# Kernel optimization log

Hardware: AMD Instinct MI355X
Metric: run time of the kernel (lower is better)

## Reference

```python
import jax, jax.numpy as jnp
import numpy as np
from jax import lax

DIM = 384
NUM_HEADS = 8
KV_NUM_HEADS = 2
REP = NUM_HEADS // KV_NUM_HEADS  # 4
KV_DIM = DIM * 2 // REP          # 192
EPS_LN = 1e-5
EPS_NORM = 1e-12


def _layernorm_channel(x, w, b):
    # WithBias LayerNorm over channel dim of NCHW tensor (matches to_3d -> LN(c) -> to_4d)
    mu = jnp.mean(x, axis=1, keepdims=True)
    var = jnp.var(x, axis=1, keepdims=True)
    return (x - mu) / jnp.sqrt(var + EPS_LN) * w[None, :, None, None] + b[None, :, None, None]


def _conv1x1(x, w):
    # w: [out, in] ; x: [b, in, h, w]
    return jnp.einsum('oi,bihw->bohw', w, x)


def _dwconv3x3(x, w):
    # depthwise 3x3, padding=1; w: [C, 1, 3, 3]
    C = x.shape[1]
    return lax.conv_general_dilated(
        x, w, window_strides=(1, 1), padding=((1, 1), (1, 1)),
        feature_group_count=C,
        dimension_numbers=('NCHW', 'OIHW', 'NCHW'))


def _l2norm(x):
    n = jnp.linalg.norm(x, axis=-1, keepdims=True)
    return x / jnp.maximum(n, EPS_NORM)


def setup_inputs() -> dict:
    key = jax.random.key(0)
    ks = jax.random.split(key, 8)
    b, h, w = 8, 128, 128
    scale1 = 1.0 / np.sqrt(DIM)
    return {
        'q': jax.random.normal(ks[0], (b, DIM, h, w), dtype=jnp.float32),
        'k': jax.random.normal(ks[1], (b, DIM, h, w), dtype=jnp.float32),
        'w_q': jax.random.normal(ks[2], (DIM, DIM), dtype=jnp.float32) * scale1,
        'w_kv': jax.random.normal(ks[3], (KV_DIM, DIM), dtype=jnp.float32) * scale1,
        'w_q_dw': jax.random.normal(ks[4], (DIM, 1, 3, 3), dtype=jnp.float32) * (1.0 / 3.0),
        'w_kv_dw': jax.random.normal(ks[5], (KV_DIM, 1, 3, 3), dtype=jnp.float32) * (1.0 / 3.0),
        'w_out': jax.random.normal(ks[6], (DIM, DIM), dtype=jnp.float32) * scale1,
        'temperature': jnp.ones((NUM_HEADS, 1, 1), dtype=jnp.float32),
        'lnq_w': jnp.ones((DIM,), dtype=jnp.float32),
        'lnq_b': jnp.zeros((DIM,), dtype=jnp.float32),
        'lnk_w': jnp.ones((DIM,), dtype=jnp.float32),
        'lnk_b': jnp.zeros((DIM,), dtype=jnp.float32),
    }


def reference(q, k, w_q, w_kv, w_q_dw, w_kv_dw, w_out, temperature,
              lnq_w, lnq_b, lnk_w, lnk_b):
    b, c, h, w = q.shape
    hw = h * w
    qn = _layernorm_channel(q, lnq_w, lnq_b)
    kn = _layernorm_channel(k, lnk_w, lnk_b)
    qp = _dwconv3x3(_conv1x1(qn, w_q), w_q_dw)          # [b, dim, h, w]
    kv = _dwconv3x3(_conv1x1(kn, w_kv), w_kv_dw)        # [b, 2*dim/rep, h, w]
    kk, vv = jnp.split(kv, 2, axis=1)                   # each [b, dim/rep, h, w]
    # reshape to heads: channel-attention layout [b, head, c_head, hw]
    qh = qp.reshape(b, NUM_HEADS, DIM // NUM_HEADS, hw)
    kh = kk.reshape(b, KV_NUM_HEADS, DIM // NUM_HEADS, hw)
    vh = vv.reshape(b, KV_NUM_HEADS, DIM // NUM_HEADS, hw)
    # GQA repeat kv heads (repeat_interleave on head dim)
    kh = jnp.repeat(kh, REP, axis=1)
    vh = jnp.repeat(vh, REP, axis=1)
    qh = _l2norm(qh)
    kh = _l2norm(kh)
    attn = jnp.einsum('bhck,bhdk->bhcd', qh, kh) * temperature[None]
    attn = jax.nn.softmax(attn, axis=-1)
    out = jnp.einsum('bhcd,bhdk->bhck', attn, vh)       # [b, head, c_head, hw]
    out = out.reshape(b, DIM, h, w)
    return _conv1x1(out, w_out)
```

## Files before the change

kernel.cpp:

```cpp
#include <hip/hip_runtime.h>
#include <math.h>


typedef unsigned short u16;
typedef unsigned int u32;
typedef short s16x8 __attribute__((ext_vector_type(8)));
typedef float f32x4 __attribute__((ext_vector_type(4)));

#define HW 16384
#define NB 8
#define CDIM 384
#define KVC 192

__device__ __forceinline__ float b2f(u16 u) {
  return __uint_as_float(((u32)u) << 16);
}
__device__ __forceinline__ u16 f2b(float f) {
  u32 u = __float_as_uint(f);
  u += 0x7fffu + ((u >> 16) & 1u);
  return (u16)(u >> 16);
}
__device__ __forceinline__ u32 pack2(float a, float c) {
  return (u32)f2b(a) | ((u32)f2b(c) << 16);
}

__global__ void k0_prep(const float* __restrict__ wq, const float* __restrict__ wkv,
                        const float* __restrict__ wo,
                        const float* __restrict__ lnqw, const float* __restrict__ lnqb,
                        const float* __restrict__ lnkw, const float* __restrict__ lnkb,
                        u16* __restrict__ wqp, float* __restrict__ rwsQ, float* __restrict__ biasQ,
                        u16* __restrict__ wkvp, float* __restrict__ rwsKV, float* __restrict__ biasKV,
                        u16* __restrict__ wop) {
  int r = blockIdx.x * 256 + threadIdx.x;
  if (r < 384) {
    float rs = 0.f, bs = 0.f;
    for (int i = 0; i < 384; ++i) {
      float wp = wq[r * 384 + i] * lnqw[i];
      u16 h = f2b(wp);
      rs += b2f(h);
      bs += wq[r * 384 + i] * lnqb[i];
      wqp[r * 384 + i] = h;
    }
    rwsQ[r] = rs; biasQ[r] = bs;
  } else if (r < 640) {
    int o = r - 384;
    if (o < 192) {
      float rs = 0.f, bs = 0.f;
      for (int i = 0; i < 384; ++i) {
        float wp = wkv[o * 384 + i] * lnkw[i];
        u16 h = f2b(wp);
        rs += b2f(h);
        bs += wkv[o * 384 + i] * lnkb[i];
        wkvp[o * 384 + i] = h;
      }
      rwsKV[o] = rs; biasKV[o] = bs;
    } else {
      for (int i = 0; i < 384; ++i) wkvp[o * 384 + i] = 0;
      rwsKV[o] = 0.f; biasKV[o] = 0.f;
    }
  } else {
    int o = r - 640;
    for (int i = 0; i < 384; ++i) wop[o * 384 + i] = f2b(wo[o * 384 + i]);
  }
}

template <int MODE, int WM, int WN, int MF, int NF>
__global__ __launch_bounds__(512, 4) void gemm_fused(const u16* __restrict__ A,
                                                     const void* __restrict__ Bsrc,
                                                     const float* __restrict__ rowsum,
                                                     const float* __restrict__ bias,
                                                     void* __restrict__ outv, int M) {
  __shared__ __align__(16) char smem[57344];
  u16*   tB    = (u16*)smem;
  float* sredS = (float*)(smem + 49152);
  float* sredQ = (float*)(smem + 53248);
  u16*   chB16 = (u16*)smem;
  float* chB32 = (float*)smem;
  __shared__ float muL[64], sdL[64];

  constexpr int M_TILE = WM * MF * 16;

  const int b = blockIdx.z;
  const int pt = ((blockIdx.x & 7) << 5) | (blockIdx.x >> 3);
  const int tid = threadIdx.x;
  const int w = tid >> 6, l = tid & 63;
  const int wm = (WN == 1) ? w : (w >> 1);
  const int wn = (WN == 1) ? 0 : (w & 1);
  const int lr = l & 15, lg = l >> 4;

  f32x4 acc[MF][NF] = {};

  if (MODE == 0) {
    const float* Bf = (const float*)Bsrc;
    const size_t fbase = (size_t)b * CDIM * HW + (size_t)pt * 64 + l;
    float v[48];
#pragma unroll
    for (int it = 0; it < 12; ++it)
#pragma unroll
      for (int j = 0; j < 4; ++j)
        v[it * 4 + j] = Bf[fbase + (size_t)(it * 32 + w * 4 + j) * HW];

    float s_ = 0.f, q_ = 0.f;
#pragma unroll
    for (int it = 0; it < 12; ++it) {
      float v0 = v[it * 4], v1 = v[it * 4 + 1], v2 = v[it * 4 + 2], v3 = v[it * 4 + 3];
      s_ += (v0 + v1) + (v2 + v3);
      q_ += (v0 * v0 + v1 * v1) + (v2 * v2 + v3 * v3);
      u32 lo = pack2(v0, v1), hi = pack2(v2, v3);
      int cidx = it * 4 + (w >> 1);
      int off = l * 384 + ((cidx ^ (l & 7)) << 3) + (w & 1) * 4;
      *(uint2*)&tB[off] = make_uint2(lo, hi);
    }
    sredS[w * 64 + l] = s_;
    sredQ[w * 64 + l] = q_;
  } else {
    const u16* Bh = (const u16*)Bsrc;
    uint4 v[6];
#pragma unroll
    for (int i = 0; i < 6; ++i) {
      int chunk = tid + i * 512;
      int row = chunk / 48, c = chunk % 48;
      v[i] = *(const uint4*)(Bh + ((size_t)(b * HW + pt * 64 + row)) * 384 + c * 8);
    }
#pragma unroll
    for (int i = 0; i < 6; ++i) {
      int chunk = tid + i * 512;
      int row = chunk / 48, c = chunk % 48;
      *(uint4*)&tB[row * 384 + ((c ^ (row & 7)) << 3)] = v[i];
    }
  }
  __syncthreads();

  if (MODE == 0) {
    if (tid < 64) {
      float s = 0.f, q2 = 0.f;
#pragma unroll
      for (int g = 0; g < 8; ++g) { s += sredS[g * 64 + tid]; q2 += sredQ[g * 64 + tid]; }
      float mn = s * (1.f / 384.f);
      float var = q2 * (1.f / 384.f) - mn * mn;
      muL[tid] = mn;
      sdL[tid] = rsqrtf(var + 1e-5f);
    }
    __syncthreads();
  }

  s16x8 a[2][MF], bb[2][NF];
  {
#pragma unroll
    for (int mf = 0; mf < MF; ++mf)
      a[0][mf] = *(const s16x8*)(A + (size_t)(wm * (MF * 16) + mf * 16 + lr) * 384 + lg * 8);
#pragma unroll
    for (int nf = 0; nf < NF; ++nf) {
      int row = wn * (NF * 16) + nf * 16 + lr;
      bb[0][nf] = *(const s16x8*)&tB[row * 384 + ((lg ^ (row & 7)) << 3)];
    }
  }
#pragma unroll
  for (int ks = 0; ks < 12; ++ks) {
    const int cur = ks & 1, nxt = cur ^ 1;
    if (ks < 11) {
      const int ko = (ks + 1) * 32 + lg * 8;
      const int cidx = (ks + 1) * 4 + lg;
#pragma unroll
      for (int mf = 0; mf < MF; ++mf)
        a[nxt][mf] = *(const s16x8*)(A + (size_t)(wm * (MF * 16) + mf * 16 + lr) * 384 + ko);
#pragma unroll
      for (int nf = 0; nf < NF; ++nf) {
        int row = wn * (NF * 16) + nf * 16 + lr;
        bb[nxt][nf] = *(const s16x8*)&tB[row * 384 + ((cidx ^ (row & 7)) << 3)];
      }
    }
#pragma unroll
    for (int mf = 0; mf < MF; ++mf)
#pragma unroll
      for (int nf = 0; nf < NF; ++nf)
        acc[mf][nf] = __builtin_amdgcn_mfma_f32_16x16x32_bf16(a[cur][mf], bb[cur][nf], acc[mf][nf], 0, 0, 0);
  }

  if (MODE == 0) {
    __syncthreads();
#pragma unroll
    for (int nf = 0; nf < NF; ++nf) {
      int prow = wn * (NF * 16) + nf * 16 + lr;
      float m_ = muL[prow], s_ = sdL[prow];
#pragma unroll
      for (int mf = 0; mf < MF; ++mf)
#pragma unroll
        for (int r = 0; r < 4; ++r) {
          int orow = wm * (MF * 16) + mf * 16 + lg * 4 + r;
          float v = s_ * (acc[mf][nf][r] - m_ * rowsum[orow]) + bias[orow];
          chB16[orow * 72 + prow] = f2b(v);
        }
    }
    __syncthreads();
    const int total = M_TILE * 8;
    for (int i = tid; i < total; i += 512) {
      int row = i >> 3, c8 = i & 7;
      uint4 v = *(const uint4*)&chB16[row * 72 + c8 * 8];
      *(uint4*)((u16*)outv + ((size_t)(b * M + row)) * HW + pt * 64 + c8 * 8) = v;
    }
  } else {
#pragma unroll
    for (int cc = 0; cc < 2; ++cc) {
      __syncthreads();
      if ((wm >> 2) == cc) {
#pragma unroll
        for (int nf = 0; nf < NF; ++nf) {
          int prow = wn * (NF * 16) + nf * 16 + lr;
#pragma unroll
          for (int mf = 0; mf < MF; ++mf)
#pragma unroll
            for (int r = 0; r < 4; ++r) {
              int orow_l = (wm & 3) * (MF * 16) + mf * 16 + lg * 4 + r;
              chB32[orow_l * 72 + prow] = acc[mf][nf][r];
            }
        }
      }
      __syncthreads();
      for (int i = tid; i < 192 * 16; i += 512) {
        int row = i >> 4, c4 = i & 15;
        uint4 v = *(const uint4*)&chB32[row * 72 + c4 * 4];
        *(uint4*)((float*)outv + ((size_t)(b * CDIM + cc * 192 + row)) * HW + pt * 64 + c4 * 4) = v;
      }
    }
  }
}

__global__ __launch_bounds__(256) void k4_dw(const u16* __restrict__ qp, const u16* __restrict__ kvp,
                                             const float* __restrict__ wqdw, const float* __restrict__ wkvdw,
                                             u16* __restrict__ qd, u16* __restrict__ kvd,
                                             float* __restrict__ rnq, float* __restrict__ rnk) {
  __shared__ u16 plane[16384];
  __shared__ float red[256];

  int c = blockIdx.x, b = blockIdx.y;
  int tid = threadIdx.x;
  const u16* in; u16* outb; const float* wp; int C;
  int isQ = (c < 384), cc = isQ ? c : c - 384;
  if (isQ) { in = qp; outb = qd; wp = wqdw + cc * 9; C = CDIM; }
  else     { in = kvp; outb = kvd; wp = wkvdw + cc * 9; C = KVC; }
  size_t base = ((size_t)(b * C + cc)) * HW;

  float w[9];
#pragma unroll
  for (int j = 0; j < 9; ++j) w[j] = wp[j];

  const uint4* gsrc = (const uint4*)(in + base);
  uint4* lplane = (uint4*)plane;
#pragma unroll
  for (int i = 0; i < 8; ++i) lplane[tid + i * 256] = gsrc[tid + i * 256];
  __syncthreads();

  uint4* gdst = (uint4*)(outb + base);
  float ns = 0.f;
#pragma unroll
  for (int it = 0; it < 8; ++it) {
    int idx = tid + it * 256;
    int y = idx >> 4, ox = idx & 15;
    int x0 = ox * 8;

    float r[3][10];
#pragma unroll
    for (int rr = 0; rr < 3; ++rr) {
      int yy = y + rr - 1;
      if ((unsigned)yy < 128u) {
        int rbase = yy * 128 + x0;
        r[rr][0] = (x0 > 0) ? b2f(plane[rbase - 1]) : 0.f;
        uint4 v = *(const uint4*)&plane[rbase];
        u32 ws[4] = {v.x, v.y, v.z, v.w};
#pragma unroll
        for (int j = 0; j < 4; ++j) {
          r[rr][1 + 2 * j] = b2f((u16)(ws[j] & 0xffff));
          r[rr][2 + 2 * j] = b2f((u16)(ws[j] >> 16));
        }
        r[rr][9] = (x0 < 120) ? b2f(plane[rbase + 8]) : 0.f;
      } else {
#pragma unroll
        for (int j = 0; j < 10; ++j) r[rr][j] = 0.f;
      }
    }

    u32 packed[4];
#pragma unroll
    for (int j = 0; j < 8; ++j) {
      float a = 0.f;
#pragma unroll
      for (int rr = 0; rr < 3; ++rr)
#pragma unroll
        for (int dx = 0; dx < 3; ++dx)
          a += w[rr * 3 + dx] * r[rr][j + dx];
      u16 h = f2b(a);
      float hv = b2f(h);
      ns += hv * hv;
      if (j & 1) packed[j >> 1] |= ((u32)h) << 16; else packed[j >> 1] = (u32)h;
    }
    gdst[idx] = make_uint4(packed[0], packed[1], packed[2], packed[3]);
  }

  red[tid] = ns;
  __syncthreads();
  for (int st = 128; st > 0; st >>= 1) {
    if (tid < st) red[tid] += red[tid + st];
    __syncthreads();
  }
  if (tid == 0) {
    float n = sqrtf(red[0]);
    float inv = 1.f / fmaxf(n, 1e-12f);
    if (isQ) rnq[b * 384 + cc] = inv;
    else if (cc < 96) rnk[b * 96 + cc] = inv;
  }
}

__global__ void k5b_vt(const u16* __restrict__ kvd, u16* __restrict__ vt) {
  int p = blockIdx.x * 256 + threadIdx.x;
  int b = blockIdx.y;
  size_t sb = ((size_t)(b * KVC + 96)) * HW + p;
  uint4* dv = (uint4*)vt + ((size_t)(b * HW + p)) * 12;
  for (int j8 = 0; j8 < 12; ++j8) {
    u32 w[4];
#pragma unroll
    for (int j = 0; j < 8; ++j) {
      u16 h = kvd[sb + (size_t)(j8 * 8 + j) * HW];
      if (j & 1) w[j >> 1] |= ((u32)h) << 16; else w[j >> 1] = (u32)h;
    }
    dv[j8] = make_uint4(w[0], w[1], w[2], w[3]);
  }
}

__global__ __launch_bounds__(256) void k6_qk(const u16* __restrict__ qd,
                                             const u16* __restrict__ kvd,
                                             float* __restrict__ spart) {
  int kc = blockIdx.x, h = blockIdx.y, b = blockIdx.z;
  int tid = threadIdx.x;
  int w = tid >> 6, l = tid & 63, lr = l & 15, lg = l >> 4;
  int g = h >> 2;
  int p0 = kc * 1024 + w * 256;

  f32x4 acc[3][3] = {};
  size_t qbase = ((size_t)(b * CDIM + h * 48 + lr)) * HW;
  size_t kbase = ((size_t)(b * KVC + g * 48 + lr)) * HW;

  for (int ks = 0; ks < 8; ++ks) {
    int pp = p0 + ks * 32 + lg * 8;
    s16x8 a[3], bb[3];
#pragma unroll
    for (int mi = 0; mi < 3; ++mi) a[mi] = *(const s16x8*)(qd + qbase + (size_t)mi * 16 * HW + pp);
#pragma unroll
    for (int ni = 0; ni < 3; ++ni) bb[ni] = *(const s16x8*)(kvd + kbase + (size_t)ni * 16 * HW + pp);
#pragma unroll
    for (int mi = 0; mi < 3; ++mi)
#pragma unroll
      for (int ni = 0; ni < 3; ++ni)
        acc[mi][ni] = __builtin_amdgcn_mfma_f32_16x16x32_bf16(a[mi], bb[ni], acc[mi][ni], 0, 0, 0);
  }

  size_t sb = ((size_t)((((b * 8 + h) * 16) + kc) * 4 + w)) * 2304;
#pragma unroll
  for (int mi = 0; mi < 3; ++mi)
#pragma unroll
    for (int ni = 0; ni < 3; ++ni)
#pragma unroll
      for (int r = 0; r < 4; ++r) {
        int c = mi * 16 + lg * 4 + r, d = ni * 16 + lr;
        spart[sb + c * 48 + d] = acc[mi][ni][r];
      }
}

__global__ void k7_sm(const float* __restrict__ spart, const float* __restrict__ temp,
                      const float* __restrict__ rnq, const float* __restrict__ rnk,
                      u16* __restrict__ ptil) {
  int h = blockIdx.x, b = blockIdx.y, tid = threadIdx.x;
  int g = h >> 2;
  __shared__ float S[2304];
  size_t base = ((size_t)((b * 8 + h) * 64)) * 2304;
  for (int e = tid; e < 2304; e += 64) {
    float s = 0.f;
    for (int j = 0; j < 64; ++j) s += spart[base + (size_t)j * 2304 + e];
    S[e] = s;
  }
  __syncthreads();
  if (tid < 48) {
    int c = tid;
    float sq = temp[h] * rnq[b * 384 + h * 48 + c];
    float mx = -1e30f;
    for (int d = 0; d < 48; ++d) {
      float v = S[c * 48 + d] * sq * rnk[b * 96 + g * 48 + d];
      mx = fmaxf(mx, v);
    }
    float sum = 0.f;
    for (int d = 0; d < 48; ++d) {
      float v = S[c * 48 + d] * sq * rnk[b * 96 + g * 48 + d];
      sum += __expf(v - mx);
    }
    float inv = 1.f / sum;
    u16* row = ptil + ((size_t)(b * 384 + h * 48 + c)) * 96;
    for (int dk = 0; dk < 96; ++dk) {
      int d = dk - g * 48;
      float pv = 0.f;
      if (d >= 0 && d < 48) {
        float v = S[c * 48 + d] * sq * rnk[b * 96 + g * 48 + d];
        pv = __expf(v - mx) * inv;
      }
      row[dk] = f2b(pv);
    }
  }
}

__global__ __launch_bounds__(512) void k8_pv(const u16* __restrict__ vt,
                                             const u16* __restrict__ ptil,
                                             u16* __restrict__ yt) {
  int ptb = blockIdx.x, b = blockIdx.y;
  int tid = threadIdx.x;
  int w = tid >> 6, l = tid & 63, lr = l & 15, lg = l >> 4;
  int wm = w >> 2, wn = w & 3;

  f32x4 acc[4][6] = {};
  size_t arow0 = ((size_t)(b * HW + ptb * 128 + wm * 64 + lr)) * 96;
  size_t brow0 = ((size_t)(b * CDIM + wn * 96 + lr)) * 96;

  for (int ks = 0; ks < 3; ++ks) {
    int ko = ks * 32 + lg * 8;
    s16x8 a[4], bb[6];
#pragma unroll
    for (int mf = 0; mf < 4; ++mf) a[mf] = *(const s16x8*)(vt + arow0 + (size_t)mf * 16 * 96 + ko);
#pragma unroll
    for (int nf = 0; nf < 6; ++nf) bb[nf] = *(const s16x8*)(ptil + brow0 + (size_t)nf * 16 * 96 + ko);
#pragma unroll
    for (int mf = 0; mf < 4; ++mf)
#pragma unroll
      for (int nf = 0; nf < 6; ++nf)
        acc[mf][nf] = __builtin_amdgcn_mfma_f32_16x16x32_bf16(a[mf], bb[nf], acc[mf][nf], 0, 0, 0);
  }

#pragma unroll
  for (int mf = 0; mf < 4; ++mf)
#pragma unroll
    for (int nf = 0; nf < 6; ++nf)
#pragma unroll
      for (int r = 0; r < 4; ++r) {
        int p = ptb * 128 + wm * 64 + mf * 16 + lg * 4 + r;
        int c = wn * 96 + nf * 16 + lr;
        yt[((size_t)(b * HW + p)) * 384 + c] = f2b(acc[mf][nf][r]);
      }
}

extern "C" void kernel_launch(void* const* d_in, const int* in_sizes, int n_in,
                              void* d_out, int out_size, void* d_ws, size_t ws_size,
                              hipStream_t stream) {
  const float* q    = (const float*)d_in[0];
  const float* k    = (const float*)d_in[1];
  const float* w_q  = (const float*)d_in[2];
  const float* w_kv = (const float*)d_in[3];
  const float* w_qd = (const float*)d_in[4];
  const float* w_kd = (const float*)d_in[5];
  const float* w_o  = (const float*)d_in[6];
  const float* temp = (const float*)d_in[7];
  const float* lnqw = (const float*)d_in[8];
  const float* lnqb = (const float*)d_in[9];
  const float* lnkw = (const float*)d_in[10];
  const float* lnkb = (const float*)d_in[11];
  float* out = (float*)d_out;

  char* ws = (char*)d_ws;
  size_t off = 0;
  auto alloc = [&](size_t bytes) -> void* {
    void* p = ws + off;
    off += (bytes + 255) & ~(size_t)255;
    return p;
  };

  u16*   wqp   = (u16*)alloc(384 * 384 * 2);
  float* rwsQ  = (float*)alloc(384 * 4);
  float* biasQ = (float*)alloc(384 * 4);
  u16*   wkvp  = (u16*)alloc(256 * 384 * 2);
  float* rwsKV = (float*)alloc(256 * 4);
  float* biasKV= (float*)alloc(256 * 4);
  u16*   wop   = (u16*)alloc(384 * 384 * 2);
  u16*   qp    = (u16*)alloc((size_t)NB * CDIM * HW * 2);
  u16*   kvp   = (u16*)alloc((size_t)NB * KVC * HW * 2);
  u16*   qd    = (u16*)alloc((size_t)NB * CDIM * HW * 2);
  u16*   kvd   = (u16*)alloc((size_t)NB * KVC * HW * 2);
  u16*   vt    = (u16*)alloc((size_t)NB * HW * 96 * 2);
  float* spart = (float*)alloc((size_t)4096 * 2304 * 4);
  u16*   ptil  = (u16*)alloc((size_t)NB * CDIM * 96 * 2);
  float* rnq   = (float*)alloc((size_t)NB * 384 * 4);
  float* rnk   = (float*)alloc((size_t)NB * 96 * 4);

  u16* yt = qp;

  k0_prep<<<4, 256, 0, stream>>>(w_q, w_kv, w_o, lnqw, lnqb, lnkw, lnkb,
                                 wqp, rwsQ, biasQ, wkvp, rwsKV, biasKV, wop);

  gemm_fused<0, 8, 1, 3, 4><<<dim3(256, 1, NB), 512, 0, stream>>>(wqp, q, rwsQ, biasQ, qp, 384);
  gemm_fused<0, 4, 2, 3, 2><<<dim3(256, 1, NB), 512, 0, stream>>>(wkvp, k, rwsKV, biasKV, kvp, 192);

  k4_dw<<<dim3(576, NB), 256, 0, stream>>>(qp, kvp, w_qd, w_kd, qd, kvd, rnq, rnk);

  k5b_vt<<<dim3(64, NB), 256, 0, stream>>>(kvd, vt);

  k6_qk<<<dim3(16, 8, NB), 256, 0, stream>>>(qd, kvd, spart);
  k7_sm<<<dim3(8, NB), 64, 0, stream>>>(spart, temp, rnq, rnk, ptil);

  k8_pv<<<dim3(128, NB), 512, 0, stream>>>(vt, ptil, yt);

  gemm_fused<1, 8, 1, 3, 4><<<dim3(256, 1, NB), 512, 0, stream>>>(wop, yt, nullptr, nullptr, out, 384);
}
```

Before: 620.3 us.

## Fuse PV product into output projection and merge Q/KV projection launches

The attention-times-V product is now computed per 64-pixel tile directly into shared memory and fed into the output 1x1 projection in the same kernel. This removes the bf16 round-trip of the intermediate yt tensor through global memory and one launch. The Q and KV projection GEMMs are merged into a single launch over 16 z-slices, with KV weights padded to 384 rows so both use the same tiling, which adds wasted MFMA work on zero rows for the KV half. The fused output kernel reloads the ptil rows from global per tile, and its larger shared-memory footprint may reduce occupancy.

Result: slower. 638.6 us (+3.0%).

```diff
diff --git a/kernel.cpp b/kernel.cpp
--- a/kernel.cpp
+++ b/kernel.cpp
@@ -42,7 +42,7 @@
       wqp[r * 384 + i] = h;
     }
     rwsQ[r] = rs; biasQ[r] = bs;
-  } else if (r < 640) {
+  } else if (r < 768) {
     int o = r - 384;
     if (o < 192) {
       float rs = 0.f, bs = 0.f;
@@ -58,40 +58,46 @@
       for (int i = 0; i < 384; ++i) wkvp[o * 384 + i] = 0;
       rwsKV[o] = 0.f; biasKV[o] = 0.f;
     }
-  } else {
-    int o = r - 640;
+  } else if (r < 1152) {
+    int o = r - 768;
     for (int i = 0; i < 384; ++i) wop[o * 384 + i] = f2b(wo[o * 384 + i]);
   }
 }
 
-template <int MODE, int WM, int WN, int MF, int NF>
-__global__ __launch_bounds__(512, 4) void gemm_fused(const u16* __restrict__ A,
-                                                     const void* __restrict__ Bsrc,
-                                                     const float* __restrict__ rowsum,
-                                                     const float* __restrict__ bias,
-                                                     void* __restrict__ outv, int M) {
-  __shared__ __align__(16) char smem[57344];
-  u16*   tB    = (u16*)smem;
-  float* sredS = (float*)(smem + 49152);
-  float* sredQ = (float*)(smem + 53248);
-  u16*   chB16 = (u16*)smem;
-  float* chB32 = (float*)smem;
-  __shared__ float muL[64], sdL[64];
-
-  constexpr int M_TILE = WM * MF * 16;
-
-  const int b = blockIdx.z;
+__global__ __launch_bounds__(512, 4) void gemm_qkv(const u16* __restrict__ Aq,
+                                                   const u16* __restrict__ Akv,
+                                                   const float* __restrict__ qsrc,
+                                                   const float* __restrict__ ksrc,
+                                                   const float* __restrict__ rwsQ,
+                                                   const float* __restrict__ biasQ,
+                                                   const float* __restrict__ rwsKV,
+                                                   const float* __restrict__ biasKV,
+                                                   u16* __restrict__ qp, u16* __restrict__ kvp) {
+  __shared__ __align__(16) char smem[53760];
+  u16*    tB   = (u16*)smem;
+  float2* sred = (float2*)(smem + 49152);
+  float*  muL  = (float*)(smem + 53248);
+  float*  sdL  = (float*)(smem + 53504);
+  u16*    chB16 = (u16*)smem;
+
+  const int zz = blockIdx.z;
+  const bool isQ = (zz < 8);
+  const int b = zz & 7;
+  const u16* A = isQ ? Aq : Akv;
+  const float* Bf = isQ ? qsrc : ksrc;
+  const float* rowsum = isQ ? rwsQ : rwsKV;
+  const float* bias = isQ ? biasQ : biasKV;
+  u16* outp = isQ ? qp : kvp;
+  const int M = isQ ? 384 : 192;
+
   const int pt = ((blockIdx.x & 7) << 5) | (blockIdx.x >> 3);
   const int tid = threadIdx.x;
   const int w = tid >> 6, l = tid & 63;
-  const int wm = (WN == 1) ? w : (w >> 1);
-  const int wn = (WN == 1) ? 0 : (w & 1);
   const int lr = l & 15, lg = l >> 4;
 
-  f32x4 acc[MF][NF] = {};
-
-  if (MODE == 0) {
-    const float* Bf = (const float*)Bsrc;
+  f32x4 acc[3][4] = {};
+
+  {
     const size_t fbase = (size_t)b * CDIM * HW + (size_t)pt * 64 + l;
     float v[48];
 #pragma unroll
@@ -111,49 +117,29 @@
       int off = l * 384 + ((cidx ^ (l & 7)) << 3) + (w & 1) * 4;
       *(uint2*)&tB[off] = make_uint2(lo, hi);
     }
-    sredS[w * 64 + l] = s_;
-    sredQ[w * 64 + l] = q_;
-  } else {
-    const u16* Bh = (const u16*)Bsrc;
-    uint4 v[6];
-#pragma unroll
-    for (int i = 0; i < 6; ++i) {
-      int chunk = tid + i * 512;
-      int row = chunk / 48, c = chunk % 48;
-      v[i] = *(const uint4*)(Bh + ((size_t)(b * HW + pt * 64 + row)) * 384 + c * 8);
-    }
-#pragma unroll
-    for (int i = 0; i < 6; ++i) {
-      int chunk = tid + i * 512;
-      int row = chunk / 48, c = chunk % 48;
-      *(uint4*)&tB[row * 384 + ((c ^ (row & 7)) << 3)] = v[i];
-    }
-  }
-  __syncthreads();
-
-  if (MODE == 0) {
-    if (tid < 64) {
-      float s = 0.f, q2 = 0.f;
-#pragma unroll
-      for (int g = 0; g < 8; ++g) { s += sredS[g * 64 + tid]; q2 += sredQ[g * 64 + tid]; }
-      float mn = s * (1.f / 384.f);
-      float var = q2 * (1.f / 384.f) - mn * mn;
-      muL[tid] = mn;
-      sdL[tid] = rsqrtf(var + 1e-5f);
-    }
-    __syncthreads();
-  }
-
-  s16x8 a[2][MF], bb[2][NF];
-  {
-#pragma unroll
-    for (int mf = 0; mf < MF; ++mf)
-      a[0][mf] = *(const s16x8*)(A + (size_t)(wm * (MF * 16) + mf * 16 + lr) * 384 + lg * 8);
-#pragma unroll
-    for (int nf = 0; nf < NF; ++nf) {
-      int row = wn * (NF * 16) + nf * 16 + lr;
-      bb[0][nf] = *(const s16x8*)&tB[row * 384 + ((lg ^ (row & 7)) << 3)];
-    }
+    sred[w * 64 + l] = make_float2(s_, q_);
+  }
+  __syncthreads();
+
+  if (tid < 64) {
+    float s = 0.f, q2 = 0.f;
+#pragma unroll
+    for (int g = 0; g < 8; ++g) { float2 t = sred[g * 64 + tid]; s += t.x; q2 += t.y; }
+    float mn = s * (1.f / 384.f);
+    float var = q2 * (1.f / 384.f) - mn * mn;
+    muL[tid] = mn;
+    sdL[tid] = rsqrtf(var + 1e-5f);
+  }
+  __syncthreads();
+
+  s16x8 a[2][3], bb[2][4];
+#pragma unroll
+  for (int mf = 0; mf < 3; ++mf)
+    a[0][mf] = *(const s16x8*)(A + (size_t)(w * 48 + mf * 16 + lr) * 384 + lg * 8);
+#pragma unroll
+  for (int nf = 0; nf < 4; ++nf) {
+    int row = nf * 16 + lr;
+    bb[0][nf] = *(const s16x8*)&tB[row * 384 + ((lg ^ (row & 7)) << 3)];
   }
 #pragma unroll
   for (int ks = 0; ks < 12; ++ks) {
@@ -162,65 +148,46 @@
       const int ko = (ks + 1) * 32 + lg * 8;
       const int cidx = (ks + 1) * 4 + lg;
 #pragma unroll
-      for (int mf = 0; mf < MF; ++mf)
-        a[nxt][mf] = *(const s16x8*)(A + (size_t)(wm * (MF * 16) + mf * 16 + lr) * 384 + ko);
-#pragma unroll
-      for (int nf = 0; nf < NF; ++nf) {
-        int row = wn * (NF * 16) + nf * 16 + lr;
+      for (int mf = 0; mf < 3; ++mf)
+        a[nxt][mf] = *(const s16x8*)(A + (size_t)(w * 48 + mf * 16 + lr) * 384 + ko);
+#pragma unroll
+      for (int nf = 0; nf < 4; ++nf) {
+        int row = nf * 16 + lr;
         bb[nxt][nf] = *(const s16x8*)&tB[row * 384 + ((cidx ^ (row & 7)) << 3)];
       }
     }
 #pragma unroll
-    for (int mf = 0; mf < MF; ++mf)
-#pragma unroll
-      for (int nf = 0; nf < NF; ++nf)
+    for (int mf = 0; mf < 3; ++mf)
+#pragma unroll
+      for (int nf = 0; nf < 4; ++nf)
         acc[mf][nf] = __builtin_amdgcn_mfma_f32_16x16x32_bf16(a[cur][mf], bb[cur][nf], acc[mf][nf], 0, 0, 0);
   }
 
-  if (MODE == 0) {
+#pragma unroll
+  for (int cc = 0; cc < 2; ++cc) {
     __syncthreads();
-#pragma unroll
-    for (int nf = 0; nf < NF; ++nf) {
-      int prow = wn * (NF * 16) + nf * 16 + lr;
-      float m_ = muL[prow], s_ = sdL[prow];
-#pragma unroll
-      for (int mf = 0; mf < MF; ++mf)
-#pragma unroll
-        for (int r = 0; r < 4; ++r) {
-          int orow = wm * (MF * 16) + mf * 16 + lg * 4 + r;
-          float v = s_ * (acc[mf][nf][r] - m_ * rowsum[orow]) + bias[orow];
-          chB16[orow * 72 + prow] = f2b(v);
-        }
+    if ((w >> 2) == cc) {
+#pragma unroll
+      for (int nf = 0; nf < 4; ++nf) {
+        int prow = nf * 16 + lr;
+        float m_ = muL[prow], s_ = sdL[prow];
+#pragma unroll
+        for (int mf = 0; mf < 3; ++mf)
+#pragma unroll
+          for (int r = 0; r < 4; ++r) {
+            int orow = w * 48 + mf * 16 + lg * 4 + r;
+            float v = s_ * (acc[mf][nf][r] - m_ * rowsum[orow]) + bias[orow];
+            chB16[((w & 3) * 48 + mf * 16 + lg * 4 + r) * 72 + prow] = f2b(v);
+          }
+      }
     }
     __syncthreads();
-    const int total = M_TILE * 8;
-    for (int i = tid; i < total; i += 512) {
+    for (int i = tid; i < 192 * 8; i += 512) {
       int row = i >> 3, c8 = i & 7;
-      uint4 v = *(const uint4*)&chB16[row * 72 + c8 * 8];
-      *(uint4*)((u16*)outv + ((size_t)(b * M + row)) * HW + pt * 64 + c8 * 8) = v;
-    }
-  } else {
-#pragma unroll
-    for (int cc = 0; cc < 2; ++cc) {
-      __syncthreads();
-      if ((wm >> 2) == cc) {
-#pragma unroll
-        for (int nf = 0; nf < NF; ++nf) {
-          int prow = wn * (NF * 16) + nf * 16 + lr;
-#pragma unroll
-          for (int mf = 0; mf < MF; ++mf)
-#pragma unroll
-            for (int r = 0; r < 4; ++r) {
-              int orow_l = (wm & 3) * (MF * 16) + mf * 16 + lg * 4 + r;
-              chB32[orow_l * 72 + prow] = acc[mf][nf][r];
-            }
-        }
-      }
-      __syncthreads();
-      for (int i = tid; i < 192 * 16; i += 512) {
-        int row = i >> 4, c4 = i & 15;
-        uint4 v = *(const uint4*)&chB32[row * 72 + c4 * 4];
-        *(uint4*)((float*)outv + ((size_t)(b * CDIM + cc * 192 + row)) * HW + pt * 64 + c4 * 4) = v;
+      int g = cc * 192 + row;
+      if (g < M) {
+        uint4 v = *(const uint4*)&chB16[row * 72 + c8 * 8];
+        *(uint4*)(outp + ((size_t)(b * M + g)) * HW + pt * 64 + c8 * 8) = v;
       }
     }
   }
@@ -406,42 +373,124 @@
   }
 }
 
-__global__ __launch_bounds__(512) void k8_pv(const u16* __restrict__ vt,
-                                             const u16* __restrict__ ptil,
-                                             u16* __restrict__ yt) {
-  int ptb = blockIdx.x, b = blockIdx.y;
-  int tid = threadIdx.x;
-  int w = tid >> 6, l = tid & 63, lr = l & 15, lg = l >> 4;
-  int wm = w >> 2, wn = w & 3;
-
-  f32x4 acc[4][6] = {};
-  size_t arow0 = ((size_t)(b * HW + ptb * 128 + wm * 64 + lr)) * 96;
-  size_t brow0 = ((size_t)(b * CDIM + wn * 96 + lr)) * 96;
-
-  for (int ks = 0; ks < 3; ++ks) {
-    int ko = ks * 32 + lg * 8;
-    s16x8 a[4], bb[6];
-#pragma unroll
-    for (int mf = 0; mf < 4; ++mf) a[mf] = *(const s16x8*)(vt + arow0 + (size_t)mf * 16 * 96 + ko);
-#pragma unroll
-    for (int nf = 0; nf < 6; ++nf) bb[nf] = *(const s16x8*)(ptil + brow0 + (size_t)nf * 16 * 96 + ko);
-#pragma unroll
-    for (int mf = 0; mf < 4; ++mf)
-#pragma unroll
-      for (int nf = 0; nf < 6; ++nf)
-        acc[mf][nf] = __builtin_amdgcn_mfma_f32_16x16x32_bf16(a[mf], bb[nf], acc[mf][nf], 0, 0, 0);
-  }
-
-#pragma unroll
-  for (int mf = 0; mf < 4; ++mf)
-#pragma unroll
-    for (int nf = 0; nf < 6; ++nf)
-#pragma unroll
-      for (int r = 0; r < 4; ++r) {
-        int p = ptb * 128 + wm * 64 + mf * 16 + lg * 4 + r;
-        int c = wn * 96 + nf * 16 + lr;
-        yt[((size_t)(b * HW + p)) * 384 + c] = f2b(acc[mf][nf][r]);
-      }
+__global__ __launch_bounds__(512, 4) void k8_out(const u16* __restrict__ vt,
+                                                 const u16* __restrict__ ptil,
+                                                 const u16* __restrict__ wop,
+                                                 float* __restrict__ out) {
+  __shared__ __align__(16) char smem[62464];
+  u16* tB = (u16*)smem;
+  u16* tV = (u16*)(smem + 49152);
+  float* chB32 = (float*)smem;
+
+  const int b = blockIdx.z;
+  const int pt = ((blockIdx.x & 7) << 5) | (blockIdx.x >> 3);
+  const int tid = threadIdx.x;
+  const int w = tid >> 6, l = tid & 63;
+  const int lr = l & 15, lg = l >> 4;
+
+  {
+    int c0 = tid;
+    int row = c0 / 12, cc = c0 % 12;
+    uint4 v = *(const uint4*)(vt + ((size_t)(b * HW + pt * 64 + row)) * 96 + cc * 8);
+    *(uint4*)&tV[row * 104 + cc * 8] = v;
+    if (tid < 256) {
+      int c1 = 512 + tid;
+      int row1 = c1 / 12, cc1 = c1 % 12;
+      uint4 v1 = *(const uint4*)(vt + ((size_t)(b * HW + pt * 64 + row1)) * 96 + cc1 * 8);
+      *(uint4*)&tV[row1 * 104 + cc1 * 8] = v1;
+    }
+  }
+  __syncthreads();
+
+  {
+    f32x4 accA[3][4] = {};
+#pragma unroll
+    for (int ks = 0; ks < 3; ++ks) {
+      s16x8 a[3], bb[4];
+#pragma unroll
+      for (int mf = 0; mf < 3; ++mf)
+        a[mf] = *(const s16x8*)(ptil + ((size_t)(b * 384 + w * 48 + mf * 16 + lr)) * 96 + ks * 32 + lg * 8);
+#pragma unroll
+      for (int nf = 0; nf < 4; ++nf)
+        bb[nf] = *(const s16x8*)&tV[(nf * 16 + lr) * 104 + ks * 32 + lg * 8];
+#pragma unroll
+      for (int mf = 0; mf < 3; ++mf)
+#pragma unroll
+        for (int nf = 0; nf < 4; ++nf)
+          accA[mf][nf] = __builtin_amdgcn_mfma_f32_16x16x32_bf16(a[mf], bb[nf], accA[mf][nf], 0, 0, 0);
+    }
+#pragma unroll
+    for (int mf = 0; mf < 3; ++mf)
+#pragma unroll
+      for (int nf = 0; nf < 4; ++nf) {
+        int prow = nf * 16 + lr;
+        int cbase = w * 48 + mf * 16 + lg * 4;
+        u32 lo = pack2(accA[mf][nf][0], accA[mf][nf][1]);
+        u32 hi = pack2(accA[mf][nf][2], accA[mf][nf][3]);
+        int chunk = (cbase >> 3) ^ (prow & 7);
+        int off = prow * 384 + chunk * 8 + (cbase & 7);
+        *(uint2*)&tB[off] = make_uint2(lo, hi);
+      }
+  }
+  __syncthreads();
+
+  f32x4 acc[3][4] = {};
+  {
+    s16x8 a[2][3], bb[2][4];
+#pragma unroll
+    for (int mf = 0; mf < 3; ++mf)
+      a[0][mf] = *(const s16x8*)(wop + (size_t)(w * 48 + mf * 16 + lr) * 384 + lg * 8);
+#pragma unroll
+    for (int nf = 0; nf < 4; ++nf) {
+      int row = nf * 16 + lr;
+      bb[0][nf] = *(const s16x8*)&tB[row * 384 + ((lg ^ (row & 7)) << 3)];
+    }
+#pragma unroll
+    for (int ks = 0; ks < 12; ++ks) {
+      const int cur = ks & 1, nxt = cur ^ 1;
+      if (ks < 11) {
+        const int ko = (ks + 1) * 32 + lg * 8;
+        const int cidx = (ks + 1) * 4 + lg;
+#pragma unroll
+        for (int mf = 0; mf < 3; ++mf)
+          a[nxt][mf] = *(const s16x8*)(wop + (size_t)(w * 48 + mf * 16 + lr) * 384 + ko);
+#pragma unroll
+        for (int nf = 0; nf < 4; ++nf) {
+          int row = nf * 16 + lr;
+          bb[nxt][nf] = *(const s16x8*)&tB[row * 384 + ((cidx ^ (row & 7)) << 3)];
+        }
+      }
+#pragma unroll
+      for (int mf = 0; mf < 3; ++mf)
+#pragma unroll
+        for (int nf = 0; nf < 4; ++nf)
+          acc[mf][nf] = __builtin_amdgcn_mfma_f32_16x16x32_bf16(a[cur][mf], bb[cur][nf], acc[mf][nf], 0, 0, 0);
+    }
+  }
+
+#pragma unroll
+  for (int cc = 0; cc < 2; ++cc) {
+    __syncthreads();
+    if ((w >> 2) == cc) {
+#pragma unroll
+      for (int nf = 0; nf < 4; ++nf) {
+        int prow = nf * 16 + lr;
+#pragma unroll
+        for (int mf = 0; mf < 3; ++mf)
+#pragma unroll
+          for (int r = 0; r < 4; ++r) {
+            int orow_l = (w & 3) * 48 + mf * 16 + lg * 4 + r;
+            chB32[orow_l * 72 + prow] = acc[mf][nf][r];
+          }
+      }
+    }
+    __syncthreads();
+    for (int i = tid; i < 192 * 16; i += 512) {
+      int row = i >> 4, c4 = i & 15;
+      uint4 v = *(const uint4*)&chB32[row * 72 + c4 * 4];
+      *(uint4*)(out + ((size_t)(b * CDIM + cc * 192 + row)) * HW + pt * 64 + c4 * 4) = v;
+    }
+  }
 }
 
 extern "C" void kernel_launch(void* const* d_in, const int* in_sizes, int n_in,
@@ -472,9 +521,9 @@
   u16*   wqp   = (u16*)alloc(384 * 384 * 2);
   float* rwsQ  = (float*)alloc(384 * 4);
   float* biasQ = (float*)alloc(384 * 4);
-  u16*   wkvp  = (u16*)alloc(256 * 384 * 2);
-  float* rwsKV = (float*)alloc(256 * 4);
-  float* biasKV= (float*)alloc(256 * 4);
+  u16*   wkvp  = (u16*)alloc(384 * 384 * 2);
+  float* rwsKV = (float*)alloc(384 * 4);
+  float* biasKV= (float*)alloc(384 * 4);
   u16*   wop   = (u16*)alloc(384 * 384 * 2);
   u16*   qp    = (u16*)alloc((size_t)NB * CDIM * HW * 2);
   u16*   kvp   = (u16*)alloc((size_t)NB * KVC * HW * 2);
@@ -486,13 +535,11 @@
   float* rnq   = (float*)alloc((size_t)NB * 384 * 4);
   float* rnk   = (float*)alloc((size_t)NB * 96 * 4);
 
-  u16* yt = qp;
-
-  k0_prep<<<4, 256, 0, stream>>>(w_q, w_kv, w_o, lnqw, lnqb, lnkw, lnkb,
+  k0_prep<<<5, 256, 0, stream>>>(w_q, w_kv, w_o, lnqw, lnqb, lnkw, lnkb,
                                  wqp, rwsQ, biasQ, wkvp, rwsKV, biasKV, wop);
 
-  gemm_fused<0, 8, 1, 3, 4><<<dim3(256, 1, NB), 512, 0, stream>>>(wqp, q, rwsQ, biasQ, qp, 384);
-  gemm_fused<0, 4, 2, 3, 2><<<dim3(256, 1, NB), 512, 0, stream>>>(wkvp, k, rwsKV, biasKV, kvp, 192);
+  gemm_qkv<<<dim3(256, 1, 16), 512, 0, stream>>>(wqp, wkvp, q, k,
+                                                 rwsQ, biasQ, rwsKV, biasKV, qp, kvp);
 
   k4_dw<<<dim3(576, NB), 256, 0, stream>>>(qp, kvp, w_qd, w_kd, qd, kvd, rnq, rnk);
 
@@ -501,7 +548,5 @@
   k6_qk<<<dim3(16, 8, NB), 256, 0, stream>>>(qd, kvd, spart);
   k7_sm<<<dim3(8, NB), 64, 0, stream>>>(spart, temp, rnq, rnk, ptil);
 
-  k8_pv<<<dim3(128, NB), 512, 0, stream>>>(vt, ptil, yt);
-
-  gemm_fused<1, 8, 1, 3, 4><<<dim3(256, 1, NB), 512, 0, stream>>>(wop, yt, nullptr, nullptr, out, 384);
-}
+  k8_out<<<dim3(256, 1, NB), 512, 0, stream>>>(vt, ptil, wop, out);
+}
```

## Fuse attention-value product with output projection in one kernel

Applied to the files above, without the earlier changes.

Replaces the separate P·V kernel and the output-projection GEMM with a single kernel. It computes the P·V tile into shared memory as bf16 and immediately multiplies it by the output weights, so the intermediate yt tensor never round-trips through global memory. It also halves the split-K partitioning in the QK kernel, which shrinks the partial-sum buffer and the reduction work in softmax at the cost of less parallelism. The fused kernel uses 1024 threads and about 126KB of LDS, which limits occupancy. The GEMM template is simplified to the LN mode only, and the kv weight padding is widened.

Result: faster. 546.2 us (-11.9%).

```diff
diff --git a/kernel.cpp b/kernel.cpp
--- a/kernel.cpp
+++ b/kernel.cpp
@@ -42,7 +42,7 @@
       wqp[r * 384 + i] = h;
     }
     rwsQ[r] = rs; biasQ[r] = bs;
-  } else if (r < 640) {
+  } else if (r < 768) {
     int o = r - 384;
     if (o < 192) {
       float rs = 0.f, bs = 0.f;
@@ -58,8 +58,8 @@
       for (int i = 0; i < 384; ++i) wkvp[o * 384 + i] = 0;
       rwsKV[o] = 0.f; biasKV[o] = 0.f;
     }
-  } else {
-    int o = r - 640;
+  } else if (r < 1152) {
+    int o = r - 768;
     for (int i = 0; i < 384; ++i) wop[o * 384 + i] = f2b(wo[o * 384 + i]);
   }
 }
@@ -75,7 +75,6 @@
   float* sredS = (float*)(smem + 49152);
   float* sredQ = (float*)(smem + 53248);
   u16*   chB16 = (u16*)smem;
-  float* chB32 = (float*)smem;
   __shared__ float muL[64], sdL[64];
 
   constexpr int M_TILE = WM * MF * 16;
@@ -90,7 +89,7 @@
 
   f32x4 acc[MF][NF] = {};
 
-  if (MODE == 0) {
+  {
     const float* Bf = (const float*)Bsrc;
     const size_t fbase = (size_t)b * CDIM * HW + (size_t)pt * 64 + l;
     float v[48];
@@ -113,47 +112,28 @@
     }
     sredS[w * 64 + l] = s_;
     sredQ[w * 64 + l] = q_;
-  } else {
-    const u16* Bh = (const u16*)Bsrc;
-    uint4 v[6];
-#pragma unroll
-    for (int i = 0; i < 6; ++i) {
-      int chunk = tid + i * 512;
-      int row = chunk / 48, c = chunk % 48;
-      v[i] = *(const uint4*)(Bh + ((size_t)(b * HW + pt * 64 + row)) * 384 + c * 8);
-    }
-#pragma unroll
-    for (int i = 0; i < 6; ++i) {
-      int chunk = tid + i * 512;
-      int row = chunk / 48, c = chunk % 48;
-      *(uint4*)&tB[row * 384 + ((c ^ (row & 7)) << 3)] = v[i];
-    }
-  }
-  __syncthreads();
-
-  if (MODE == 0) {
-    if (tid < 64) {
-      float s = 0.f, q2 = 0.f;
-#pragma unroll
-      for (int g = 0; g < 8; ++g) { s += sredS[g * 64 + tid]; q2 += sredQ[g * 64 + tid]; }
-      float mn = s * (1.f / 384.f);
-      float var = q2 * (1.f / 384.f) - mn * mn;
-      muL[tid] = mn;
-      sdL[tid] = rsqrtf(var + 1e-5f);
-    }
-    __syncthreads();
-  }
+  }
+  __syncthreads();
+
+  if (tid < 64) {
+    float s = 0.f, q2 = 0.f;
+#pragma unroll
+    for (int g = 0; g < 8; ++g) { s += sredS[g * 64 + tid]; q2 += sredQ[g * 64 + tid]; }
+    float mn = s * (1.f / 384.f);
+    float var = q2 * (1.f / 384.f) - mn * mn;
+    muL[tid] = mn;
+    sdL[tid] = rsqrtf(var + 1e-5f);
+  }
+  __syncthreads();
 
   s16x8 a[2][MF], bb[2][NF];
-  {
-#pragma unroll
-    for (int mf = 0; mf < MF; ++mf)
-      a[0][mf] = *(const s16x8*)(A + (size_t)(wm * (MF * 16) + mf * 16 + lr) * 384 + lg * 8);
-#pragma unroll
-    for (int nf = 0; nf < NF; ++nf) {
-      int row = wn * (NF * 16) + nf * 16 + lr;
-      bb[0][nf] = *(const s16x8*)&tB[row * 384 + ((lg ^ (row & 7)) << 3)];
-    }
+#pragma unroll
+  for (int mf = 0; mf < MF; ++mf)
+    a[0][mf] = *(const s16x8*)(A + (size_t)(wm * (MF * 16) + mf * 16 + lr) * 384 + lg * 8);
+#pragma unroll
+  for (int nf = 0; nf < NF; ++nf) {
+    int row = wn * (NF * 16) + nf * 16 + lr;
+    bb[0][nf] = *(const s16x8*)&tB[row * 384 + ((lg ^ (row & 7)) << 3)];
   }
 #pragma unroll
   for (int ks = 0; ks < 12; ++ks) {
@@ -177,51 +157,27 @@
         acc[mf][nf] = __builtin_amdgcn_mfma_f32_16x16x32_bf16(a[cur][mf], bb[cur][nf], acc[mf][nf], 0, 0, 0);
   }
 
-  if (MODE == 0) {
-    __syncthreads();
-#pragma unroll
-    for (int nf = 0; nf < NF; ++nf) {
-      int prow = wn * (NF * 16) + nf * 16 + lr;
-      float m_ = muL[prow], s_ = sdL[prow];
-#pragma unroll
-      for (int mf = 0; mf < MF; ++mf)
-#pragma unroll
-        for (int r = 0; r < 4; ++r) {
-          int orow = wm * (MF * 16) + mf * 16 + lg * 4 + r;
-          float v = s_ * (acc[mf][nf][r] - m_ * rowsum[orow]) + bias[orow];
-          chB16[orow * 72 + prow] = f2b(v);
-        }
-    }
-    __syncthreads();
-    const int total = M_TILE * 8;
-    for (int i = tid; i < total; i += 512) {
-      int row = i >> 3, c8 = i & 7;
+  __syncthreads();
+#pragma unroll
+  for (int nf = 0; nf < NF; ++nf) {
+    int prow = wn * (NF * 16) + nf * 16 + lr;
+    float m_ = muL[prow], s_ = sdL[prow];
+#pragma unroll
+    for (int mf = 0; mf < MF; ++mf)
+#pragma unroll
+      for (int r = 0; r < 4; ++r) {
+        int orow = wm * (MF * 16) + mf * 16 + lg * 4 + r;
+        float v = s_ * (acc[mf][nf][r] - m_ * rowsum[orow]) + bias[orow];
+        chB16[orow * 72 + prow] = f2b(v);
+      }
+  }
+  __syncthreads();
+  const int total = M_TILE * 8;
+  for (int i = tid; i < total; i += 512) {
+    int row = i >> 3, c8 = i & 7;
+    if (row < M) {
       uint4 v = *(const uint4*)&chB16[row * 72 + c8 * 8];
       *(uint4*)((u16*)outv + ((size_t)(b * M + row)) * HW + pt * 64 + c8 * 8) = v;
-    }
-  } else {
-#pragma unroll
-    for (int cc = 0; cc < 2; ++cc) {
-      __syncthreads();
-      if ((wm >> 2) == cc) {
-#pragma unroll
-        for (int nf = 0; nf < NF; ++nf) {
-          int prow = wn * (NF * 16) + nf * 16 + lr;
-#pragma unroll
-          for (int mf = 0; mf < MF; ++mf)
-#pragma unroll
-            for (int r = 0; r < 4; ++r) {
-              int orow_l = (wm & 3) * (MF * 16) + mf * 16 + lg * 4 + r;
-              chB32[orow_l * 72 + prow] = acc[mf][nf][r];
-            }
-        }
-      }
-      __syncthreads();
-      for (int i = tid; i < 192 * 16; i += 512) {
-        int row = i >> 4, c4 = i & 15;
-        uint4 v = *(const uint4*)&chB32[row * 72 + c4 * 4];
-        *(uint4*)((float*)outv + ((size_t)(b * CDIM + cc * 192 + row)) * HW + pt * 64 + c4 * 4) = v;
-      }
     }
   }
 }
@@ -334,13 +290,13 @@
   int tid = threadIdx.x;
   int w = tid >> 6, l = tid & 63, lr = l & 15, lg = l >> 4;
   int g = h >> 2;
-  int p0 = kc * 1024 + w * 256;
+  int p0 = kc * 2048 + w * 512;
 
   f32x4 acc[3][3] = {};
   size_t qbase = ((size_t)(b * CDIM + h * 48 + lr)) * HW;
   size_t kbase = ((size_t)(b * KVC + g * 48 + lr)) * HW;
 
-  for (int ks = 0; ks < 8; ++ks) {
+  for (int ks = 0; ks < 16; ++ks) {
     int pp = p0 + ks * 32 + lg * 8;
     s16x8 a[3], bb[3];
 #pragma unroll
@@ -354,7 +310,7 @@
         acc[mi][ni] = __builtin_amdgcn_mfma_f32_16x16x32_bf16(a[mi], bb[ni], acc[mi][ni], 0, 0, 0);
   }
 
-  size_t sb = ((size_t)((((b * 8 + h) * 16) + kc) * 4 + w)) * 2304;
+  size_t sb = ((size_t)((((b * 8 + h) * 8) + kc) * 4 + w)) * 2304;
 #pragma unroll
   for (int mi = 0; mi < 3; ++mi)
 #pragma unroll
@@ -372,10 +328,10 @@
   int h = blockIdx.x, b = blockIdx.y, tid = threadIdx.x;
   int g = h >> 2;
   __shared__ float S[2304];
-  size_t base = ((size_t)((b * 8 + h) * 64)) * 2304;
+  size_t base = ((size_t)((b * 8 + h) * 32)) * 2304;
   for (int e = tid; e < 2304; e += 64) {
     float s = 0.f;
-    for (int j = 0; j < 64; ++j) s += spart[base + (size_t)j * 2304 + e];
+    for (int j = 0; j < 32; ++j) s += spart[base + (size_t)j * 2304 + e];
     S[e] = s;
   }
   __syncthreads();
@@ -406,42 +362,124 @@
   }
 }
 
-__global__ __launch_bounds__(512) void k8_pv(const u16* __restrict__ vt,
-                                             const u16* __restrict__ ptil,
-                                             u16* __restrict__ yt) {
-  int ptb = blockIdx.x, b = blockIdx.y;
-  int tid = threadIdx.x;
-  int w = tid >> 6, l = tid & 63, lr = l & 15, lg = l >> 4;
-  int wm = w >> 2, wn = w & 3;
-
-  f32x4 acc[4][6] = {};
-  size_t arow0 = ((size_t)(b * HW + ptb * 128 + wm * 64 + lr)) * 96;
-  size_t brow0 = ((size_t)(b * CDIM + wn * 96 + lr)) * 96;
-
-  for (int ks = 0; ks < 3; ++ks) {
-    int ko = ks * 32 + lg * 8;
-    s16x8 a[4], bb[6];
-#pragma unroll
-    for (int mf = 0; mf < 4; ++mf) a[mf] = *(const s16x8*)(vt + arow0 + (size_t)mf * 16 * 96 + ko);
-#pragma unroll
-    for (int nf = 0; nf < 6; ++nf) bb[nf] = *(const s16x8*)(ptil + brow0 + (size_t)nf * 16 * 96 + ko);
-#pragma unroll
-    for (int mf = 0; mf < 4; ++mf)
-#pragma unroll
-      for (int nf = 0; nf < 6; ++nf)
-        acc[mf][nf] = __builtin_amdgcn_mfma_f32_16x16x32_bf16(a[mf], bb[nf], acc[mf][nf], 0, 0, 0);
-  }
-
-#pragma unroll
-  for (int mf = 0; mf < 4; ++mf)
-#pragma unroll
-    for (int nf = 0; nf < 6; ++nf)
-#pragma unroll
-      for (int r = 0; r < 4; ++r) {
-        int p = ptb * 128 + wm * 64 + mf * 16 + lg * 4 + r;
-        int c = wn * 96 + nf * 16 + lr;
-        yt[((size_t)(b * HW + p)) * 384 + c] = f2b(acc[mf][nf][r]);
-      }
+__global__ __launch_bounds__(1024, 4) void k8_out(const u16* __restrict__ vt,
+                                                  const u16* __restrict__ ptil,
+                                                  const u16* __restrict__ wop,
+                                                  float* __restrict__ out) {
+  __shared__ __align__(16) char smem[125952];
+  u16* tB = (u16*)smem;
+  u16* tV = (u16*)(smem + 98304);
+  float* chB32 = (float*)smem;
+
+  const int b = blockIdx.z;
+  const int pt = ((blockIdx.x & 7) << 4) | (blockIdx.x >> 3);
+  const int tid = threadIdx.x;
+  const int w = tid >> 6, l = tid & 63;
+  const int wm = w >> 1, wn = w & 1;
+  const int lr = l & 15, lg = l >> 4;
+
+  {
+#pragma unroll
+    for (int i = 0; i < 2; ++i) {
+      int c0 = tid + i * 1024;
+      if (c0 < 1536) {
+        int row = c0 / 12, cc = c0 % 12;
+        uint4 v = *(const uint4*)(vt + ((size_t)(b * HW + pt * 128 + row)) * 96 + cc * 8);
+        *(uint4*)&tV[row * 104 + cc * 8] = v;
+      }
+    }
+  }
+  __syncthreads();
+
+  {
+    f32x4 accA[3][4] = {};
+#pragma unroll
+    for (int ks = 0; ks < 3; ++ks) {
+      s16x8 a[3], bb[4];
+#pragma unroll
+      for (int mf = 0; mf < 3; ++mf)
+        a[mf] = *(const s16x8*)(ptil + ((size_t)(b * 384 + wm * 48 + mf * 16 + lr)) * 96 + ks * 32 + lg * 8);
+#pragma unroll
+      for (int nf = 0; nf < 4; ++nf)
+        bb[nf] = *(const s16x8*)&tV[(wn * 64 + nf * 16 + lr) * 104 + ks * 32 + lg * 8];
+#pragma unroll
+      for (int mf = 0; mf < 3; ++mf)
+#pragma unroll
+        for (int nf = 0; nf < 4; ++nf)
+          accA[mf][nf] = __builtin_amdgcn_mfma_f32_16x16x32_bf16(a[mf], bb[nf], accA[mf][nf], 0, 0, 0);
+    }
+#pragma unroll
+    for (int mf = 0; mf < 3; ++mf)
+#pragma unroll
+      for (int nf = 0; nf < 4; ++nf) {
+        int prow = wn * 64 + nf * 16 + lr;
+        int cbase = wm * 48 + mf * 16 + lg * 4;
+        u32 lo = pack2(accA[mf][nf][0], accA[mf][nf][1]);
+        u32 hi = pack2(accA[mf][nf][2], accA[mf][nf][3]);
+        int chunk = (cbase >> 3) ^ ((prow >> 1) & 7);
+        int off = prow * 384 + chunk * 8 + (cbase & 7);
+        *(uint2*)&tB[off] = make_uint2(lo, hi);
+      }
+  }
+  __syncthreads();
+
+  f32x4 acc[3][4] = {};
+  {
+    s16x8 a[2][3], bb[2][4];
+#pragma unroll
+    for (int mf = 0; mf < 3; ++mf)
+      a[0][mf] = *(const s16x8*)(wop + (size_t)(wm * 48 + mf * 16 + lr) * 384 + lg * 8);
+#pragma unroll
+    for (int nf = 0; nf < 4; ++nf) {
+      int row = wn * 64 + nf * 16 + lr;
+      bb[0][nf] = *(const s16x8*)&tB[row * 384 + ((lg ^ ((row >> 1) & 7)) << 3)];
+    }
+#pragma unroll
+    for (int ks = 0; ks < 12; ++ks) {
+      const int cur = ks & 1, nxt = cur ^ 1;
+      if (ks < 11) {
+        const int ko = (ks + 1) * 32 + lg * 8;
+        const int cidx = (ks + 1) * 4 + lg;
+#pragma unroll
+        for (int mf = 0; mf < 3; ++mf)
+          a[nxt][mf] = *(const s16x8*)(wop + (size_t)(wm * 48 + mf * 16 + lr) * 384 + ko);
+#pragma unroll
+        for (int nf = 0; nf < 4; ++nf) {
+          int row = wn * 64 + nf * 16 + lr;
+          bb[nxt][nf] = *(const s16x8*)&tB[row * 384 + ((cidx ^ ((row >> 1) & 7)) << 3)];
+        }
+      }
+#pragma unroll
+      for (int mf = 0; mf < 3; ++mf)
+#pragma unroll
+        for (int nf = 0; nf < 4; ++nf)
+          acc[mf][nf] = __builtin_amdgcn_mfma_f32_16x16x32_bf16(a[cur][mf], bb[cur][nf], acc[mf][nf], 0, 0, 0);
+    }
+  }
+
+#pragma unroll
+  for (int cc = 0; cc < 2; ++cc) {
+    __syncthreads();
+    if ((wm >> 2) == cc) {
+#pragma unroll
+      for (int nf = 0; nf < 4; ++nf) {
+        int prow = wn * 64 + nf * 16 + lr;
+#pragma unroll
+        for (int mf = 0; mf < 3; ++mf)
+#pragma unroll
+          for (int r = 0; r < 4; ++r) {
+            int orow_l = (wm & 3) * 48 + mf * 16 + lg * 4 + r;
+            chB32[orow_l * 132 + prow] = acc[mf][nf][r];
+          }
+      }
+    }
+    __syncthreads();
+    for (int i = tid; i < 192 * 32; i += 1024) {
+      int row = i >> 5, c4 = i & 31;
+      uint4 v = *(const uint4*)&chB32[row * 132 + c4 * 4];
+      *(uint4*)(out + ((size_t)(b * CDIM + cc * 192 + row)) * HW + pt * 128 + c4 * 4) = v;
+    }
+  }
 }
 
 extern "C" void kernel_launch(void* const* d_in, const int* in_sizes, int n_in,
@@ -472,23 +510,21 @@
   u16*   wqp   = (u16*)alloc(384 * 384 * 2);
   float* rwsQ  = (float*)alloc(384 * 4);
   float* biasQ = (float*)alloc(384 * 4);
-  u16*   wkvp  = (u16*)alloc(256 * 384 * 2);
-  float* rwsKV = (float*)alloc(256 * 4);
-  float* biasKV= (float*)alloc(256 * 4);
+  u16*   wkvp  = (u16*)alloc(384 * 384 * 2);
+  float* rwsKV = (float*)alloc(384 * 4);
+  float* biasKV= (float*)alloc(384 * 4);
   u16*   wop   = (u16*)alloc(384 * 384 * 2);
   u16*   qp    = (u16*)alloc((size_t)NB * CDIM * HW * 2);
   u16*   kvp   = (u16*)alloc((size_t)NB * KVC * HW * 2);
   u16*   qd    = (u16*)alloc((size_t)NB * CDIM * HW * 2);
   u16*   kvd   = (u16*)alloc((size_t)NB * KVC * HW * 2);
   u16*   vt    = (u16*)alloc((size_t)NB * HW * 96 * 2);
-  float* spart = (float*)alloc((size_t)4096 * 2304 * 4);
+  float* spart = (float*)alloc((size_t)2048 * 2304 * 4);
   u16*   ptil  = (u16*)alloc((size_t)NB * CDIM * 96 * 2);
   float* rnq   = (float*)alloc((size_t)NB * 384 * 4);
   float* rnk   = (float*)alloc((size_t)NB * 96 * 4);
 
-  u16* yt = qp;
-
-  k0_prep<<<4, 256, 0, stream>>>(w_q, w_kv, w_o, lnqw, lnqb, lnkw, lnkb,
+  k0_prep<<<5, 256, 0, stream>>>(w_q, w_kv, w_o, lnqw, lnqb, lnkw, lnkb,
                                  wqp, rwsQ, biasQ, wkvp, rwsKV, biasKV, wop);
 
   gemm_fused<0, 8, 1, 3, 4><<<dim3(256, 1, NB), 512, 0, stream>>>(wqp, q, rwsQ, biasQ, qp, 384);
@@ -498,10 +534,8 @@
 
   k5b_vt<<<dim3(64, NB), 256, 0, stream>>>(kvd, vt);
 
-  k6_qk<<<dim3(16, 8, NB), 256, 0, stream>>>(qd, kvd, spart);
+  k6_qk<<<dim3(8, 8, NB), 256, 0, stream>>>(qd, kvd, spart);
   k7_sm<<<dim3(8, NB), 64, 0, stream>>>(spart, temp, rnq, rnk, ptil);
 
-  k8_pv<<<dim3(128, NB), 512, 0, stream>>>(vt, ptil, yt);
-
-  gemm_fused<1, 8, 1, 3, 4><<<dim3(256, 1, NB), 512, 0, stream>>>(wop, yt, nullptr, nullptr, out, 384);
-}
+  k8_out<<<dim3(128, 1, NB), 1024, 0, stream>>>(vt, ptil, wop, out);
+}
```
